# Kernel tuning notes

Measured on AMD Instinct MI355X. Metric: run time of the kernel, lower is better.

The kernel has to match this reference:

```python
import jax, jax.numpy as jnp
import numpy as np

B, N, PAST = 2, 1024, 1024
DIM, HEADS, DH = 2048, 16, 128
INNER = HEADS * DH
LN_EPS = 1e-5
ROPE_THETA = 10000.0


def setup_inputs() -> dict:
    key = jax.random.key(0)
    k0, k1, k2, k3, k4 = jax.random.split(key, 5)
    x = jax.random.normal(k0, (B, N, DIM), dtype=jnp.float32)
    past_k = jax.random.normal(k1, (B, HEADS, PAST, DH), dtype=jnp.float32)
    past_v = jax.random.normal(k2, (B, HEADS, PAST, DH), dtype=jnp.float32)
    # causal mask with KV-cache offset: query i sits at global pos PAST+i,
    # mask (True = blocked) keys at positions j > PAST+i
    kv = PAST + N
    q_pos = PAST + jnp.arange(N)
    k_pos = jnp.arange(kv)
    mask = jnp.broadcast_to((k_pos[None, :] > q_pos[:, None])[None, None], (B, 1, N, kv))
    w_qkv = jax.random.normal(k3, (DIM, 3 * INNER), dtype=jnp.float32) * (DIM ** -0.5)
    w_out = jax.random.normal(k4, (INNER, DIM), dtype=jnp.float32) * (INNER ** -0.5)
    ln_g = jnp.ones((DIM,), dtype=jnp.float32)
    ln_b = jnp.zeros((DIM,), dtype=jnp.float32)
    return {"x": x, "past_k": past_k, "past_v": past_v, "mask": mask,
            "w_qkv": w_qkv, "w_out": w_out, "ln_g": ln_g, "ln_b": ln_b}


def _layernorm(x, g, b):
    mu = jnp.mean(x, axis=-1, keepdims=True)
    var = jnp.mean((x - mu) ** 2, axis=-1, keepdims=True)
    return (x - mu) * jax.lax.rsqrt(var + LN_EPS) * g + b


def _rope(t, pos):
    # interleaved rotary (lucidrains rotary-embedding-torch convention)
    inv_freq = 1.0 / (ROPE_THETA ** (jnp.arange(0, DH, 2, dtype=jnp.float32) / DH))
    freqs = pos.astype(jnp.float32)[:, None] * inv_freq[None, :]   # [n, DH/2]
    freqs = jnp.repeat(freqs, 2, axis=-1)                          # [n, DH]
    cos = jnp.cos(freqs).astype(t.dtype)
    sin = jnp.sin(freqs).astype(t.dtype)
    t2 = t.reshape(*t.shape[:-1], DH // 2, 2)
    rot = jnp.stack((-t2[..., 1], t2[..., 0]), axis=-1).reshape(t.shape)
    return t * cos + rot * sin


def reference(x, past_k, past_v, mask, w_qkv, w_out, ln_g, ln_b):
    b, n, _ = x.shape
    xn = _layernorm(x, ln_g, ln_b)
    qkv = xn @ w_qkv                                               # [b, n, 3*INNER]
    q, k, v = jnp.split(qkv, 3, axis=-1)
    to_heads = lambda t: t.reshape(b, n, HEADS, DH).transpose(0, 2, 1, 3)  # b h n d
    q, k, v = to_heads(q), to_heads(k), to_heads(v)
    k = jnp.concatenate((past_k, k), axis=2)                       # [b, h, kv, d]
    v = jnp.concatenate((past_v, v), axis=2)
    kv_len = k.shape[2]
    q = _rope(q, jnp.arange(n) + (kv_len - n))
    k = _rope(k, jnp.arange(kv_len))
    scale = DH ** -0.5
    dots = jnp.einsum('bhnd,bhmd->bhnm', q, k) * scale             # [b, h, n, kv]
    dots = jnp.where(mask, -jnp.inf, dots)
    attn = jax.nn.softmax(dots, axis=-1)
    out = jnp.einsum('bhnm,bhmd->bhnd', attn, v)                   # [b, h, n, d]
    out = out.transpose(0, 2, 1, 3).reshape(b, n, INNER)
    return out @ w_out, k, v
```

## Files before the change

kernel.cpp:

```cpp
#include <hip/hip_runtime.h>
#include <hip/hip_bf16.h>
#include <math.h>

#define BB    2
#define NN    1024
#define PAST  1024
#define KVL   2048
#define DIM   2048
#define HEADS 16
#define DH    128
#define INNER 2048
#define NQKV  6144
#define TOK   2048
#define LN_EPS 1e-5f

typedef __attribute__((ext_vector_type(8)))  short    short8;
typedef __attribute__((ext_vector_type(4)))  float    f32x4;
typedef __attribute__((ext_vector_type(16))) float    f32x16;
typedef __attribute__((ext_vector_type(8)))  unsigned short us8;
typedef __attribute__((ext_vector_type(4)))  unsigned short us4;
typedef unsigned short us;

__device__ __forceinline__ float bfbits2f(us u) {
    return __uint_as_float(((unsigned int)u) << 16);
}
__device__ __forceinline__ us f2bfb(float f) {
    union { __hip_bfloat16 h; us u; } cv;
    cv.h = __float2bfloat16(f);
    return cv.u;
}
__device__ __forceinline__ unsigned pkbf(float a, float b) {
    return (unsigned)f2bfb(a) | ((unsigned)f2bfb(b) << 16);
}
__device__ __forceinline__ us8 pack8u(float4 a, float4 b) {
    us8 r;
    r[0] = f2bfb(a.x); r[1] = f2bfb(a.y); r[2] = f2bfb(a.z); r[3] = f2bfb(a.w);
    r[4] = f2bfb(b.x); r[5] = f2bfb(b.y); r[6] = f2bfb(b.z); r[7] = f2bfb(b.w);
    return r;
}

__device__ __forceinline__ void gload_lds16(const void* gsrc, void* ldst) {
    __builtin_amdgcn_global_load_lds(
        (const __attribute__((address_space(1))) void*)gsrc,
        (__attribute__((address_space(3))) void*)ldst, 16, 0, 0);
}

__global__ __launch_bounds__(256) void transp_kernel(
    const float* __restrict__ src, us* __restrict__ dst, int R, int C)
{
    const int c0 = blockIdx.x * 64;
    const int r0 = blockIdx.y * 64;
    const int tid = threadIdx.x;

    __shared__ us T[64][68];

    #pragma unroll
    for (int e = 0; e < 4; e++) {
        int idx = tid + e * 256;
        int jr  = idx >> 4;
        int c4  = (idx & 15) * 4;
        float4 v = *reinterpret_cast<const float4*>(
            src + (size_t)(r0 + jr) * C + c0 + c4);
        us4 w;
        w[0] = f2bfb(v.x); w[1] = f2bfb(v.y); w[2] = f2bfb(v.z); w[3] = f2bfb(v.w);
        *reinterpret_cast<us4*>(&T[jr][c4]) = w;
    }
    __syncthreads();

    #pragma unroll
    for (int e = 0; e < 4; e++) {
        int idx = tid + e * 256;
        int d   = idx >> 4;
        int k4  = (idx & 15) * 4;
        us4 w;
        w[0] = T[k4 + 0][d];
        w[1] = T[k4 + 1][d];
        w[2] = T[k4 + 2][d];
        w[3] = T[k4 + 3][d];
        *reinterpret_cast<us4*>(dst + (size_t)(c0 + d) * R + r0 + k4) = w;
    }
}

__global__ __launch_bounds__(256) void ln_kernel(
    const float* __restrict__ x, const float* __restrict__ g,
    const float* __restrict__ b, us* __restrict__ xn)
{
    const int t   = blockIdx.x;
    const int tid = threadIdx.x;
    const size_t base = (size_t)t * DIM;

    float4 p0 = reinterpret_cast<const float4*>(x + base)[tid * 2 + 0];
    float4 p1 = reinterpret_cast<const float4*>(x + base)[tid * 2 + 1];
    float v[8] = {p0.x, p0.y, p0.z, p0.w, p1.x, p1.y, p1.z, p1.w};

    float s1 = 0.f, s2 = 0.f;
    #pragma unroll
    for (int i = 0; i < 8; i++) { s1 += v[i]; s2 += v[i] * v[i]; }

    #pragma unroll
    for (int off = 32; off; off >>= 1) {
        s1 += __shfl_xor(s1, off);
        s2 += __shfl_xor(s2, off);
    }
    __shared__ float red1[4], red2[4];
    if ((tid & 63) == 0) { red1[tid >> 6] = s1; red2[tid >> 6] = s2; }
    __syncthreads();
    float S1 = red1[0] + red1[1] + red1[2] + red1[3];
    float S2 = red2[0] + red2[1] + red2[2] + red2[3];
    const float inv = 1.0f / (float)DIM;
    float mu  = S1 * inv;
    float var = S2 * inv - mu * mu;
    float rstd = rsqrtf(var + LN_EPS);

    const int d0 = tid * 8;
    float4 oa, ob;
    oa.x = (v[0] - mu) * rstd * g[d0 + 0] + b[d0 + 0];
    oa.y = (v[1] - mu) * rstd * g[d0 + 1] + b[d0 + 1];
    oa.z = (v[2] - mu) * rstd * g[d0 + 2] + b[d0 + 2];
    oa.w = (v[3] - mu) * rstd * g[d0 + 3] + b[d0 + 3];
    ob.x = (v[4] - mu) * rstd * g[d0 + 4] + b[d0 + 4];
    ob.y = (v[5] - mu) * rstd * g[d0 + 5] + b[d0 + 5];
    ob.z = (v[6] - mu) * rstd * g[d0 + 6] + b[d0 + 6];
    ob.w = (v[7] - mu) * rstd * g[d0 + 7] + b[d0 + 7];

    *reinterpret_cast<us8*>(xn + base + d0) = pack8u(oa, ob);
}

template<bool OUT_BF16>
__global__ __launch_bounds__(256) void gemm_bt_kernel(
    const us* __restrict__ A, const us* __restrict__ Bt,
    void* __restrict__ Cout, int M, int N, int K)
{
    __shared__ us As[3][128 * 32];
    __shared__ us Bs[3][128 * 32];

    const int tid  = threadIdx.x;
    const int wave = tid >> 6, lane = tid & 63;
    const int quad = lane >> 4, l16 = lane & 15;
    const int wm = wave & 1, wn = wave >> 1;
    const int m0 = blockIdx.y * 128, n0 = blockIdx.x * 128;

    f32x4 acc[4][4];
    #pragma unroll
    for (int i = 0; i < 4; i++)
        #pragma unroll
        for (int j = 0; j < 4; j++)
            #pragma unroll
            for (int r = 0; r < 4; r++) acc[i][j][r] = 0.f;

    auto stage = [&](int k0, int buf) {
        #pragma unroll
        for (int e = 0; e < 2; e++) {
            int phys = (e * 256 + tid) * 16;
            int lr   = phys >> 7;
            int offp = (phys & 127) ^ ((lr & 7) << 4);
            int m    = 2 * lr + (offp >> 6);
            int kb   = offp & 63;
            gload_lds16((const char*)(A + (size_t)(m0 + m) * K + k0) + kb,
                        (char*)&As[buf][0] + phys);
            gload_lds16((const char*)(Bt + (size_t)(n0 + m) * K + k0) + kb,
                        (char*)&Bs[buf][0] + phys);
        }
    };

    const int ns = K >> 5;
    stage(0, 0);
    stage(32, 1);
    __builtin_amdgcn_sched_barrier(0);
    asm volatile("s_waitcnt vmcnt(4)" ::: "memory");
    __builtin_amdgcn_s_barrier();
    __builtin_amdgcn_sched_barrier(0);

    int cur = 0;
    for (int ks = 0; ks < ns; ks++) {
        if (ks + 2 < ns) stage((ks + 2) * 32, (ks + 2) % 3);

        short8 af[4], bf[4];
        #pragma unroll
        for (int mi = 0; mi < 4; mi++) {
            int mrow = wm * 64 + mi * 16 + l16;
            int lr   = mrow >> 1;
            int off  = ((mrow & 1) * 64 + quad * 16) ^ ((lr & 7) << 4);
            af[mi] = *reinterpret_cast<const short8*>(
                (const char*)&As[cur][0] + lr * 128 + off);
        }
        #pragma unroll
        for (int ni = 0; ni < 4; ni++) {
            int nrow = wn * 64 + ni * 16 + l16;
            int lr   = nrow >> 1;
            int off  = ((nrow & 1) * 64 + quad * 16) ^ ((lr & 7) << 4);
            bf[ni] = *reinterpret_cast<const short8*>(
                (const char*)&Bs[cur][0] + lr * 128 + off);
        }

        __builtin_amdgcn_s_setprio(1);
        #pragma unroll
        for (int mi = 0; mi < 4; mi++)
            #pragma unroll
            for (int ni = 0; ni < 4; ni++)
                acc[mi][ni] = __builtin_amdgcn_mfma_f32_16x16x32_bf16(
                    af[mi], bf[ni], acc[mi][ni], 0, 0, 0);
        __builtin_amdgcn_s_setprio(0);

        __builtin_amdgcn_sched_barrier(0);
        if (ks + 2 < ns) asm volatile("s_waitcnt vmcnt(4)" ::: "memory");
        else             asm volatile("s_waitcnt vmcnt(0)" ::: "memory");
        __builtin_amdgcn_s_barrier();
        __builtin_amdgcn_sched_barrier(0);
        cur = (cur == 2) ? 0 : cur + 1;
    }

    #pragma unroll
    for (int mi = 0; mi < 4; mi++) {
        #pragma unroll
        for (int r = 0; r < 4; r++) {
            size_t row = (size_t)(m0 + wm * 64 + mi * 16 + quad * 4 + r);
            #pragma unroll
            for (int ni = 0; ni < 4; ni++) {
                size_t col = n0 + wn * 64 + ni * 16 + l16;
                if (OUT_BF16)
                    ((us*)Cout)[row * N + col] = f2bfb(acc[mi][ni][r]);
                else
                    ((float*)Cout)[row * N + col] = acc[mi][ni][r];
            }
        }
    }
}

__global__ __launch_bounds__(256) void rope_kernel(
    const float* __restrict__ past_k, const float* __restrict__ past_v,
    us* __restrict__ qkv, float* __restrict__ out_k, float* __restrict__ out_v,
    us* __restrict__ Kbf)
{
    const int tid  = threadIdx.x;
    const int pid  = blockIdx.x * 4 + (tid >> 6);
    const int lane = tid & 63;

    const int b   = pid / (HEADS * KVL);
    const int rem = pid - b * (HEADS * KVL);
    const int h   = rem / KVL;
    const int pos = rem - h * KVL;

    const float invf = exp2f((float)lane * (-13.287712379549449f / 64.0f));
    float sn, cs;
    sincosf((float)pos * invf, &sn, &cs);

    const size_t obase = ((size_t)(b * HEADS + h) * KVL + pos) * DH + 2 * lane;

    float k0, k1;
    if (pos < PAST) {
        const size_t pbase = ((size_t)(b * HEADS + h) * PAST + pos) * DH + 2 * lane;
        k0 = past_k[pbase];
        k1 = past_k[pbase + 1];
    } else {
        const int t = b * NN + (pos - PAST);
        const us* qp = qkv + (size_t)t * NQKV + INNER + h * DH + 2 * lane;
        k0 = bfbits2f(qp[0]); k1 = bfbits2f(qp[1]);
    }
    float kr0 = k0 * cs - k1 * sn;
    float kr1 = k1 * cs + k0 * sn;
    out_k[obase]     = kr0;
    out_k[obase + 1] = kr1;
    Kbf[obase]       = f2bfb(kr0);
    Kbf[obase + 1]   = f2bfb(kr1);

    if (pos < PAST) {
        const size_t pbase = ((size_t)(b * HEADS + h) * PAST + pos) * DH + 2 * lane;
        out_v[obase]     = past_v[pbase];
        out_v[obase + 1] = past_v[pbase + 1];
    } else {
        const int t = b * NN + (pos - PAST);
        const us* vp = qkv + (size_t)t * NQKV + 2 * INNER + h * DH + 2 * lane;
        out_v[obase]     = bfbits2f(vp[0]);
        out_v[obase + 1] = bfbits2f(vp[1]);
    }

    if (pos >= PAST) {
        const int t = b * NN + (pos - PAST);
        us* qq = qkv + (size_t)t * NQKV + h * DH + 2 * lane;
        float q0 = bfbits2f(qq[0]), q1 = bfbits2f(qq[1]);
        qq[0] = f2bfb(q0 * cs - q1 * sn);
        qq[1] = f2bfb(q1 * cs + q0 * sn);
    }
}

__global__ __launch_bounds__(256) void vtrans_kernel(
    const float* __restrict__ Vc, us* __restrict__ Vtg)
{
    const int jb = blockIdx.x;
    const int db = blockIdx.y;
    const int bh = blockIdx.z;
    const int tid = threadIdx.x;

    __shared__ us T[64][68];

    const float* src = Vc + ((size_t)bh * KVL + jb * 64) * DH + db * 64;
    #pragma unroll
    for (int e = 0; e < 4; e++) {
        int idx = tid + e * 256;
        int jr  = idx >> 4;
        int c4  = (idx & 15) * 4;
        float4 v = *reinterpret_cast<const float4*>(src + (size_t)jr * DH + c4);
        us4 w;
        w[0] = f2bfb(v.x); w[1] = f2bfb(v.y); w[2] = f2bfb(v.z); w[3] = f2bfb(v.w);
        *reinterpret_cast<us4*>(&T[jr][c4]) = w;
    }
    __syncthreads();

    us* dst = Vtg + ((size_t)bh * DH + db * 64) * KVL + jb * 64;
    #pragma unroll
    for (int e = 0; e < 4; e++) {
        int idx = tid + e * 256;
        int d   = idx >> 4;
        int k4  = (idx & 15) * 4;
        us4 w;
        w[0] = T[k4 + 0][d];
        w[1] = T[k4 + 1][d];
        w[2] = T[k4 + 2][d];
        w[3] = T[k4 + 3][d];
        *reinterpret_cast<us4*>(dst + (size_t)d * KVL + k4) = w;
    }
}

__global__ __launch_bounds__(256) void attn_mfma_kernel(
    const us* __restrict__ qkv,
    const us* __restrict__ Kbf,
    const us* __restrict__ Vtg,
    us* __restrict__ Ao)
{
    const int tid  = threadIdx.x;
    const int wave = tid >> 6;
    const int lane = tid & 63;
    const int l32  = lane & 31;
    const int g    = lane >> 5;

    const int flat = blockIdx.x;
    const int s    = flat >> 3;
    const int grp  = (flat & 7) + 8 * (s & 3);
    const int p    = s >> 2;
    const int h    = grp & 15;
    const int b    = grp >> 4;
    const int qtile = (wave < 2) ? p : (15 - p);
    const int qsub  = (wave & 1) * 32;
    const int mynch = 17 + qtile;
    const int nch   = 32 - p;

    __shared__ us Ks[3][64 * 128];
    __shared__ us Vt[3][128 * 64];

    short8 qf[8];
    {
        const int qrow = qtile * 64 + qsub + l32;
        const us* qp = qkv + (size_t)(b * NN + qrow) * NQKV + h * DH;
        #pragma unroll
        for (int ks = 0; ks < 8; ks++)
            qf[ks] = *reinterpret_cast<const short8*>(qp + ks * 16 + g * 8);
    }

    f32x16 Oacc[4];
    #pragma unroll
    for (int dt = 0; dt < 4; dt++)
        #pragma unroll
        for (int r = 0; r < 16; r++) Oacc[dt][r] = 0.f;
    float m_run  = -INFINITY;
    float l_part = 0.f;

    const us* kptr = Kbf + (size_t)(b * HEADS + h) * KVL * DH;
    const us* vtb  = Vtg + (size_t)(b * HEADS + h) * DH * KVL;
    const float scale = 0.08838834764831845f;
    const float THRU  = 90.50966799f;
    const int qg = PAST + qtile * 64 + qsub + l32;

    auto stage = [&](int j0, int buf) {
        #pragma unroll
        for (int e = 0; e < 4; e++) {
            int phys = (e * 256 + tid) * 16;
            int row  = phys >> 8;
            int col  = (phys & 255) ^ ((row & 7) << 4);
            gload_lds16((const char*)(kptr + (size_t)(j0 + row) * DH) + col,
                        (char*)&Ks[buf][0] + phys);
        }
        #pragma unroll
        for (int e = 0; e < 4; e++) {
            int phys = (e * 256 + tid) * 16;
            int row  = phys >> 7;
            int col  = (phys & 127) ^ ((row & 7) << 4);
            gload_lds16((const char*)(vtb + (size_t)row * KVL) + j0 * 2 + col,
                        (char*)&Vt[buf][0] + phys);
        }
    };

    stage(0, 0);
    stage(64, 1);
    __builtin_amdgcn_sched_barrier(0);
    asm volatile("s_waitcnt vmcnt(8)" ::: "memory");
    __builtin_amdgcn_s_barrier();
    __builtin_amdgcn_sched_barrier(0);

    int cur = 0;
    for (int c = 0; c < nch; c++) {
        const int j0 = c * 64;
        if (c + 2 < nch) stage(j0 + 128, (c + 2) % 3 == 0 ? 0 : ((c + 2) % 3));

        if (c < mynch) {
            f32x16 S[2];
            #pragma unroll
            for (int t = 0; t < 2; t++)
                #pragma unroll
                for (int r = 0; r < 16; r++) S[t][r] = 0.f;

            __builtin_amdgcn_s_setprio(1);
            #pragma unroll
            for (int ks = 0; ks < 8; ks++) {
                #pragma unroll
                for (int t = 0; t < 2; t++) {
                    int row  = t * 32 + l32;
                    int colb = ks * 32 + g * 16;
                    const char* kp = (const char*)&Ks[cur][0] +
                                     row * 256 + (colb ^ ((row & 7) << 4));
                    short8 kb = *reinterpret_cast<const short8*>(kp);
                    S[t] = __builtin_amdgcn_mfma_f32_32x32x16_bf16(
                        kb, qf[ks], S[t], 0, 0, 0);
                }
            }
            __builtin_amdgcn_s_setprio(0);

            const int rel = qg - j0;
            float mx = -INFINITY;
            #pragma unroll
            for (int t = 0; t < 2; t++)
                #pragma unroll
                for (int r = 0; r < 16; r++) {
                    int kvo = t * 32 + (r & 3) + 8 * (r >> 2) + 4 * g;
                    S[t][r] = (kvo <= rel) ? S[t][r] : -INFINITY;
                    mx = fmaxf(mx, S[t][r]);
                }
            mx = fmaxf(mx, __shfl_xor(mx, 32));

            float alpha = 1.f;
            if (__any(mx > m_run + THRU)) {
                float nm = fmaxf(m_run, mx);
                alpha = __expf((m_run - nm) * scale);
                m_run = nm;
                #pragma unroll
                for (int r = 0; r < 16; r++) {
                    float ar = __shfl(alpha, (r & 3) + 8 * (r >> 2) + 4 * g);
                    Oacc[0][r] *= ar; Oacc[1][r] *= ar;
                    Oacc[2][r] *= ar; Oacc[3][r] *= ar;
                }
            }

            const float nmk = -m_run * scale;
            float rs = 0.f;
            #pragma unroll
            for (int t = 0; t < 2; t++)
                #pragma unroll
                for (int r = 0; r < 16; r++) {
                    float pv = __expf(fmaf(S[t][r], scale, nmk));
                    S[t][r] = pv;
                    rs += pv;
                }
            l_part = l_part * alpha + rs;

            short8 paf[4];
            #pragma unroll
            for (int t = 0; t < 2; t++)
                #pragma unroll
                for (int u = 0; u < 2; u++) {
                    unsigned cA = pkbf(S[t][8*u + 0], S[t][8*u + 1]);
                    unsigned cB = pkbf(S[t][8*u + 2], S[t][8*u + 3]);
                    unsigned dA = pkbf(S[t][8*u + 4], S[t][8*u + 5]);
                    unsigned dB = pkbf(S[t][8*u + 6], S[t][8*u + 7]);
                    asm volatile("v_permlane32_swap_b32 %0, %1"
                                 : "+v"(cA), "+v"(dA));
                    asm volatile("v_permlane32_swap_b32 %0, %1"
                                 : "+v"(cB), "+v"(dB));
                    union { unsigned u4[4]; short8 s8; } fb;
                    fb.u4[0] = cA; fb.u4[1] = cB; fb.u4[2] = dA; fb.u4[3] = dB;
                    paf[t * 2 + u] = fb.s8;
                }

            __builtin_amdgcn_s_setprio(1);
            #pragma unroll
            for (int ks = 0; ks < 4; ks++) {
                #pragma unroll
                for (int dt = 0; dt < 4; dt++) {
                    int row  = dt * 32 + l32;
                    int colb = ks * 32 + g * 16;
                    const char* vp = (const char*)&Vt[cur][0] +
                                     row * 128 + (colb ^ ((row & 7) << 4));
                    short8 vb = *reinterpret_cast<const short8*>(vp);
                    Oacc[dt] = __builtin_amdgcn_mfma_f32_32x32x16_bf16(
                        paf[ks], vb, Oacc[dt], 0, 0, 0);
                }
            }
            __builtin_amdgcn_s_setprio(0);
        }

        __builtin_amdgcn_sched_barrier(0);
        if (c + 2 < nch) asm volatile("s_waitcnt vmcnt(8)" ::: "memory");
        else             asm volatile("s_waitcnt vmcnt(0)" ::: "memory");
        __builtin_amdgcn_s_barrier();
        __builtin_amdgcn_sched_barrier(0);
        cur = (cur == 2) ? 0 : cur + 1;
    }

    l_part += __shfl_xor(l_part, 32);
    float linv = 1.f / l_part;
    #pragma unroll
    for (int r = 0; r < 16; r++) {
        int qr = (r & 3) + 8 * (r >> 2) + 4 * g;
        float iv = __shfl(linv, qr);
        int qrow = qtile * 64 + qsub + qr;
        us* dst = Ao + (size_t)(b * NN + qrow) * INNER + h * DH + l32;
        #pragma unroll
        for (int dt = 0; dt < 4; dt++)
            dst[dt * 32] = f2bfb(Oacc[dt][r] * iv);
    }
}

extern "C" void kernel_launch(void* const* d_in, const int* in_sizes, int n_in,
                              void* d_out, int out_size, void* d_ws, size_t ws_size,
                              hipStream_t stream)
{
    const float* x      = (const float*)d_in[0];
    const float* past_k = (const float*)d_in[1];
    const float* past_v = (const float*)d_in[2];
    const float* w_qkv  = (const float*)d_in[4];
    const float* w_out  = (const float*)d_in[5];
    const float* ln_g   = (const float*)d_in[6];
    const float* ln_b   = (const float*)d_in[7];

    float* out   = (float*)d_out;
    float* out_k = out   + (size_t)BB * NN * DIM;
    float* out_v = out_k + (size_t)BB * HEADS * KVL * DH;

    us* xn   = (us*)d_ws;
    us* qkv  = xn  + (size_t)TOK * DIM;
    us* Wqt  = qkv + (size_t)TOK * NQKV;
    us* Wot  = Wqt + (size_t)NQKV * DIM;
    us* Vtg  = Wot + (size_t)DIM * INNER;
    us* attn = xn;
    us* Kbf  = Wqt;

    transp_kernel<<<dim3(NQKV / 64, DIM / 64), 256, 0, stream>>>(
        w_qkv, Wqt, DIM, NQKV);
    transp_kernel<<<dim3(DIM / 64, INNER / 64), 256, 0, stream>>>(
        w_out, Wot, INNER, DIM);

    ln_kernel<<<TOK, 256, 0, stream>>>(x, ln_g, ln_b, xn);

    gemm_bt_kernel<true><<<dim3(NQKV / 128, TOK / 128), 256, 0, stream>>>(
        xn, Wqt, (void*)qkv, TOK, NQKV, DIM);

    rope_kernel<<<(BB * HEADS * KVL) / 4, 256, 0, stream>>>(
        past_k, past_v, qkv, out_k, out_v, Kbf);

    vtrans_kernel<<<dim3(KVL / 64, DH / 64, BB * HEADS), 256, 0, stream>>>(
        out_v, Vtg);

    attn_mfma_kernel<<<256, 256, 0, stream>>>(
        qkv, Kbf, Vtg, attn);

    gemm_bt_kernel<false><<<dim3(DIM / 128, TOK / 128), 256, 0, stream>>>(
        attn, Wot, (void*)out, TOK, DIM, INNER);
}
```

Measured before the change: 392.6 us.

## Use double-buffered K/V staging, 16-row swizzle, and skip masking on full chunks

Cuts the K/V LDS staging from three buffers to two, halving prefetch depth to one chunk ahead with a full vmcnt(0) wait each iteration. The V tile is re-laid out as 64 rows of 256 bytes with an XOR swizzle over 16 rows (also applied to K), to reduce LDS bank conflicts on the MFMA operand reads. Causal masking is now only applied on chunks that straddle the diagonal. Less LDS may allow more resident blocks, but the shallower prefetch risks exposing global load latency.

```diff
diff --git a/kernel.cpp b/kernel.cpp
--- a/kernel.cpp
+++ b/kernel.cpp
@@ -345,8 +345,8 @@
     const int mynch = 17 + qtile;
     const int nch   = 32 - p;
 
-    __shared__ us Ks[3][64 * 128];
-    __shared__ us Vt[3][128 * 64];
+    __shared__ us Ks[2][64 * 128];
+    __shared__ us Vt[2][64 * 128];
 
     short8 qf[8];
     {
@@ -369,38 +369,39 @@
     const us* vtb  = Vtg + (size_t)(b * HEADS + h) * DH * KVL;
     const float scale = 0.08838834764831845f;
     const float THRU  = 90.50966799f;
-    const int qg = PAST + qtile * 64 + qsub + l32;
+    const int qgmin = PAST + qtile * 64 + qsub;
+    const int qg    = qgmin + l32;
 
     auto stage = [&](int j0, int buf) {
         #pragma unroll
         for (int e = 0; e < 4; e++) {
             int phys = (e * 256 + tid) * 16;
             int row  = phys >> 8;
-            int col  = (phys & 255) ^ ((row & 7) << 4);
+            int col  = (phys & 255) ^ ((row & 15) << 4);
             gload_lds16((const char*)(kptr + (size_t)(j0 + row) * DH) + col,
                         (char*)&Ks[buf][0] + phys);
         }
         #pragma unroll
         for (int e = 0; e < 4; e++) {
             int phys = (e * 256 + tid) * 16;
-            int row  = phys >> 7;
-            int col  = (phys & 127) ^ ((row & 7) << 4);
-            gload_lds16((const char*)(vtb + (size_t)row * KVL) + j0 * 2 + col,
+            int row  = phys >> 8;
+            int offp = (phys & 255) ^ ((row & 15) << 4);
+            int d    = row + 64 * (offp >> 7);
+            int cb   = offp & 127;
+            gload_lds16((const char*)(vtb + (size_t)d * KVL) + j0 * 2 + cb,
                         (char*)&Vt[buf][0] + phys);
         }
     };
 
     stage(0, 0);
-    stage(64, 1);
-    __builtin_amdgcn_sched_barrier(0);
-    asm volatile("s_waitcnt vmcnt(8)" ::: "memory");
+    asm volatile("s_waitcnt vmcnt(0)" ::: "memory");
     __builtin_amdgcn_s_barrier();
     __builtin_amdgcn_sched_barrier(0);
 
     int cur = 0;
     for (int c = 0; c < nch; c++) {
         const int j0 = c * 64;
-        if (c + 2 < nch) stage(j0 + 128, (c + 2) % 3 == 0 ? 0 : ((c + 2) % 3));
+        if (c + 1 < nch) stage(j0 + 64, cur ^ 1);
 
         if (c < mynch) {
             f32x16 S[2];
@@ -417,7 +418,7 @@
                     int row  = t * 32 + l32;
                     int colb = ks * 32 + g * 16;
                     const char* kp = (const char*)&Ks[cur][0] +
-                                     row * 256 + (colb ^ ((row & 7) << 4));
+                                     row * 256 + (colb ^ ((row & 15) << 4));
                     short8 kb = *reinterpret_cast<const short8*>(kp);
                     S[t] = __builtin_amdgcn_mfma_f32_32x32x16_bf16(
                         kb, qf[ks], S[t], 0, 0, 0);
@@ -425,16 +426,21 @@
             }
             __builtin_amdgcn_s_setprio(0);
 
-            const int rel = qg - j0;
+            if (j0 + 63 > qgmin) {
+                const int rel = qg - j0;
+                #pragma unroll
+                for (int t = 0; t < 2; t++)
+                    #pragma unroll
+                    for (int r = 0; r < 16; r++) {
+                        int kvo = t * 32 + (r & 3) + 8 * (r >> 2) + 4 * g;
+                        S[t][r] = (kvo <= rel) ? S[t][r] : -INFINITY;
+                    }
+            }
             float mx = -INFINITY;
             #pragma unroll
             for (int t = 0; t < 2; t++)
                 #pragma unroll
-                for (int r = 0; r < 16; r++) {
-                    int kvo = t * 32 + (r & 3) + 8 * (r >> 2) + 4 * g;
-                    S[t][r] = (kvo <= rel) ? S[t][r] : -INFINITY;
-                    mx = fmaxf(mx, S[t][r]);
-                }
+                for (int r = 0; r < 16; r++) mx = fmaxf(mx, S[t][r]);
             mx = fmaxf(mx, __shfl_xor(mx, 32));
 
             float alpha = 1.f;
@@ -485,10 +491,12 @@
             for (int ks = 0; ks < 4; ks++) {
                 #pragma unroll
                 for (int dt = 0; dt < 4; dt++) {
-                    int row  = dt * 32 + l32;
-                    int colb = ks * 32 + g * 16;
+                    int d    = dt * 32 + l32;
+                    int lr   = d & 63;
+                    int off  = (((d >> 6) << 7) + ks * 32 + g * 16)
+                               ^ ((lr & 15) << 4);
                     const char* vp = (const char*)&Vt[cur][0] +
-                                     row * 128 + (colb ^ ((row & 7) << 4));
+                                     lr * 256 + off;
                     short8 vb = *reinterpret_cast<const short8*>(vp);
                     Oacc[dt] = __builtin_amdgcn_mfma_f32_32x32x16_bf16(
                         paf[ks], vb, Oacc[dt], 0, 0, 0);
@@ -498,11 +506,10 @@
         }
 
         __builtin_amdgcn_sched_barrier(0);
-        if (c + 2 < nch) asm volatile("s_waitcnt vmcnt(8)" ::: "memory");
-        else             asm volatile("s_waitcnt vmcnt(0)" ::: "memory");
+        asm volatile("s_waitcnt vmcnt(0)" ::: "memory");
         __builtin_amdgcn_s_barrier();
         __builtin_amdgcn_sched_barrier(0);
-        cur = (cur == 2) ? 0 : cur + 1;
+        cur ^= 1;
     }
 
     l_part += __shfl_xor(l_part, 32);
```

New measurement: 388.4 us. Within noise of the previous version (-1.1%).
